# Kernel optimization log

Measured on AMD Instinct MI355X. Metric: run time of the kernel, lower is better.

The kernel has to match this reference:

```python
import jax, jax.numpy as jnp
import numpy as np

D_MODEL = 1024
N_HEADS = 16
D_HEAD = D_MODEL // N_HEADS
RANK = 128
N_COMPRESS = 64
STATE_DIM = 64
B_SZ = 2
S_LEN = 2048


def setup_inputs() -> dict:
    key = jax.random.key(0)
    ks = jax.random.split(key, 12)
    x = jax.random.normal(ks[0], (B_SZ, S_LEN, D_MODEL), dtype=jnp.float32)
    A = jax.random.normal(ks[1], (STATE_DIM, STATE_DIM), dtype=jnp.float32) * 0.01
    B_ssm = jax.random.normal(ks[2], (D_MODEL, STATE_DIM), dtype=jnp.float32) * 0.01
    W_imp = jax.random.normal(ks[3], (D_MODEL, STATE_DIM), dtype=jnp.float32) * 0.02   # Linear(state_dim->d_model), weight [out,in]
    W_router = jax.random.normal(ks[4], (N_COMPRESS, D_MODEL), dtype=jnp.float32) * 0.02
    compress_neurons = jax.random.normal(ks[5], (N_COMPRESS, D_MODEL, RANK), dtype=jnp.float32) * 0.02
    Wq = jax.random.normal(ks[6], (D_MODEL, RANK), dtype=jnp.float32) * 0.02
    Wk = jax.random.normal(ks[7], (D_MODEL, RANK), dtype=jnp.float32) * 0.02
    Wv = jax.random.normal(ks[8], (D_MODEL, RANK), dtype=jnp.float32) * 0.02
    Wo = jax.random.normal(ks[9], (D_MODEL, D_MODEL), dtype=jnp.float32) * 0.02
    mask = jnp.tril(jnp.ones((S_LEN, S_LEN), dtype=bool))[None, None]  # [1,1,S,S] causal
    return {"x": x, "A": A, "B_ssm": B_ssm, "W_imp": W_imp, "W_router": W_router,
            "compress_neurons": compress_neurons, "Wq": Wq, "Wk": Wk, "Wv": Wv,
            "Wo": Wo, "mask": mask}


def reference(x, A, B_ssm, W_imp, W_router, compress_neurons, Wq, Wk, Wv, Wo, mask):
    Bn, S, D = x.shape
    # ---- SSM: h_t = h_{t-1} @ A + x_t @ B (only final state is used) ----
    xB = jnp.einsum('bsd,dn->bsn', x, B_ssm)  # precompute input projection

    def step(h, u):
        h = h @ A + u
        return h, None

    h0 = jnp.zeros((Bn, STATE_DIM), dtype=x.dtype)
    h_final, _ = jax.lax.scan(step, h0, jnp.swapaxes(xB, 0, 1))  # scan over S

    h_proj = h_final @ W_imp.T                       # [B, d_model]
    importance = jax.nn.softmax(jnp.einsum('bsd,bd->bs', x, h_proj), axis=-1)

    # ---- Routing ----
    token_pref = jax.nn.softmax(x @ W_router.T, axis=-1)          # [B,S,n_compress]
    nw = jnp.einsum('bs,bsn->bn', importance, token_pref)         # [B,n_compress]
    nw = nw / (nw.sum(axis=-1, keepdims=True) + 1e-8)

    # ---- Shared compression -> QKV ----
    shared_compress = jnp.einsum('bn,ndr->bdr', nw, compress_neurons)  # [B,D,rank]
    hcomp = jnp.einsum('bsd,bdr->bsr', x, shared_compress)             # [B,S,rank]
    Q = (hcomp @ Wq.T).reshape(Bn, S, N_HEADS, D_HEAD).transpose(0, 2, 1, 3)
    K = (hcomp @ Wk.T).reshape(Bn, S, N_HEADS, D_HEAD).transpose(0, 2, 1, 3)
    V = (hcomp @ Wv.T).reshape(Bn, S, N_HEADS, D_HEAD).transpose(0, 2, 1, 3)

    scores = jnp.einsum('bhqd,bhkd->bhqk', Q, K) / np.sqrt(D_HEAD).astype(x.dtype)
    scores = jnp.where(mask, scores, jnp.array(-jnp.inf, dtype=scores.dtype))
    attn = jax.nn.softmax(scores, axis=-1)
    attn_out = jnp.einsum('bhqk,bhkd->bhqd', attn, V)
    attn_out = attn_out.transpose(0, 2, 1, 3).reshape(Bn, S, D_MODEL)
    output = attn_out @ Wo.T
    return output
```

## Files before the change

### kernel.cpp

```cpp
#include <hip/hip_runtime.h>
#include <hip/hip_bf16.h>

typedef __bf16 bf16x8 __attribute__((ext_vector_type(8)));
typedef float  f32x4  __attribute__((ext_vector_type(4)));
typedef float  f32x16 __attribute__((ext_vector_type(16)));
typedef unsigned int uint4v __attribute__((ext_vector_type(4)));

__device__ __forceinline__ unsigned short f2bf(float f){
  union { float f; unsigned int u; } v; v.f = f;
  unsigned int r = (v.u + 0x7FFFu + ((v.u >> 16) & 1u)) >> 16;
  return (unsigned short)r;
}

__device__ __forceinline__ float bf2f(unsigned short u){
  union { unsigned int i; float f; } v; v.i = ((unsigned int)u) << 16; return v.f;
}

__device__ __forceinline__ unsigned pkbf(float a, float b){
  unsigned r;
  asm("v_cvt_pk_bf16_f32 %0, %1, %2" : "=v"(r) : "v"(a), "v"(b));
  return r;
}

__device__ __forceinline__ void gload_lds16(const void* g, void* l){
  __builtin_amdgcn_global_load_lds(
      (const __attribute__((address_space(1))) unsigned int*)g,
      (__attribute__((address_space(3))) unsigned int*)l, 16, 0, 0);
}

#define MFMA16(a,b,c) __builtin_amdgcn_mfma_f32_16x16x32_bf16((a),(b),(c),0,0,0)
#define MFMA32(a,b,c) __builtin_amdgcn_mfma_f32_32x32x16_bf16((a),(b),(c),0,0,0)

__global__ void k_conv(const float* __restrict__ x,
                       const float* __restrict__ Wq, const float* __restrict__ Wk,
                       const float* __restrict__ Wv, const float* __restrict__ Wo,
                       const float* __restrict__ Wr,
                       unsigned short* __restrict__ xb16,
                       unsigned short* __restrict__ wqkv, unsigned short* __restrict__ wo,
                       unsigned short* __restrict__ wrt){
  int bid = blockIdx.x;
  if (bid < 4096){
    int i = (bid * 256 + threadIdx.x) * 4;
    float4 v = *reinterpret_cast<const float4*>(x + i);
    ushort4 r; r.x = f2bf(v.x); r.y = f2bf(v.y); r.z = f2bf(v.z); r.w = f2bf(v.w);
    *reinterpret_cast<ushort4*>(xb16 + i) = r;
    return;
  }
  int j = ((bid - 4096) * 256 + threadIdx.x) * 4;
  if (j < 393216){
    const float* s;
    if (j < 131072) s = Wq + j; else if (j < 262144) s = Wk + (j - 131072); else s = Wv + (j - 262144);
    float4 v = *reinterpret_cast<const float4*>(s);
    ushort4 r; r.x = f2bf(v.x); r.y = f2bf(v.y); r.z = f2bf(v.z); r.w = f2bf(v.w);
    *reinterpret_cast<ushort4*>(wqkv + j) = r;
  } else if (j < 1441792){
    int jj = j - 393216;
    float4 v = *reinterpret_cast<const float4*>(Wo + jj);
    ushort4 r; r.x = f2bf(v.x); r.y = f2bf(v.y); r.z = f2bf(v.z); r.w = f2bf(v.w);
    *reinterpret_cast<ushort4*>(wo + jj) = r;
  } else {
    int jj = j - 1441792;
    int n = jj >> 10, d = jj & 1023;
    ushort4 r;
    if (n < 64){
      float4 v = *reinterpret_cast<const float4*>(Wr + n * 1024 + d);
      r.x = f2bf(v.x); r.y = f2bf(v.y); r.z = f2bf(v.z); r.w = f2bf(v.w);
    } else { r.x = 0; r.y = 0; r.z = 0; r.w = 0; }
    *reinterpret_cast<ushort4*>(wrt + jj) = r;
  }
}

template<int CBF16>
__global__ __launch_bounds__(256) void k_gemm(
    const unsigned short* __restrict__ A, const unsigned short* __restrict__ Bt,
    void* __restrict__ Cv, int M, int N, int K,
    long sA, long sB, long sC)
{
  __shared__ __align__(16) unsigned short Al[128 * 64];
  __shared__ __align__(16) unsigned short Bl[128 * 64];
  const int tid = threadIdx.x, wv = tid >> 6, lane = tid & 63;
  const int bm = blockIdx.y * 128, bn = blockIdx.x * 128, z = blockIdx.z;
  const unsigned short* Ab = A + (long)z * sA;
  const unsigned short* Bb = Bt + (long)z * sB;
  const f32x4 zero = {0.f, 0.f, 0.f, 0.f};
  f32x4 acc[4][4];
  #pragma unroll
  for (int i = 0; i < 4; ++i)
    #pragma unroll
    for (int j = 0; j < 4; ++j) acc[i][j] = zero;
  const int mo = (wv & 1) * 64, no = (wv >> 1) * 64;

  for (int k0 = 0; k0 < K; k0 += 64){
    __syncthreads();
    #pragma unroll
    for (int i = 0; i < 4; ++i){
      int rr = (wv * 4 + i) * 8 + (lane >> 3);
      gload_lds16(Ab + (long)(bm + rr) * K + k0 + (lane & 7) * 8, &Al[(wv * 4 + i) * 8 * 64]);
      gload_lds16(Bb + (long)(bn + rr) * K + k0 + (lane & 7) * 8, &Bl[(wv * 4 + i) * 8 * 64]);
    }
    __syncthreads();
    #pragma unroll
    for (int ks = 0; ks < 2; ++ks){
      bf16x8 af[4], bfr[4];
      #pragma unroll
      for (int mi = 0; mi < 4; ++mi)
        af[mi] = *reinterpret_cast<const bf16x8*>(&Al[(mo + mi * 16 + (lane & 15)) * 64 + ks * 32 + (lane >> 4) * 8]);
      #pragma unroll
      for (int ni = 0; ni < 4; ++ni)
        bfr[ni] = *reinterpret_cast<const bf16x8*>(&Bl[(no + ni * 16 + (lane & 15)) * 64 + ks * 32 + (lane >> 4) * 8]);
      #pragma unroll
      for (int mi = 0; mi < 4; ++mi)
        #pragma unroll
        for (int ni = 0; ni < 4; ++ni)
          acc[mi][ni] = MFMA16(af[mi], bfr[ni], acc[mi][ni]);
    }
  }

  #pragma unroll
  for (int mi = 0; mi < 4; ++mi)
    #pragma unroll
    for (int ni = 0; ni < 4; ++ni)
      #pragma unroll
      for (int r = 0; r < 4; ++r){
        int row = bm + mo + mi * 16 + (lane >> 4) * 4 + r;
        int col = bn + no + ni * 16 + (lane & 15);
        float v = acc[mi][ni][r];
        if (CBF16) ((unsigned short*)Cv)[(long)z * sC + (long)row * N + col] = f2bf(v);
        else       ((float*)Cv)[(long)z * sC + (long)row * N + col] = v;
      }
}

__global__ __launch_bounds__(256) void k_gemm64(
    const unsigned short* __restrict__ A, const unsigned short* __restrict__ Bt,
    float* __restrict__ C, int M, int N, int K)
{
  __shared__ __align__(16) unsigned short Al[128 * 64];
  __shared__ __align__(16) unsigned short Bl[64 * 64];
  const int tid = threadIdx.x, wv = tid >> 6, lane = tid & 63;
  const int bm = blockIdx.y * 128, bn = blockIdx.x * 64;
  const f32x4 zero = {0.f, 0.f, 0.f, 0.f};
  f32x4 acc[4][2];
  #pragma unroll
  for (int i = 0; i < 4; ++i){ acc[i][0] = zero; acc[i][1] = zero; }
  const int mo = (wv & 1) * 64, no = (wv >> 1) * 32;

  for (int k0 = 0; k0 < K; k0 += 64){
    __syncthreads();
    #pragma unroll
    for (int i = 0; i < 4; ++i){
      int rr = (wv * 4 + i) * 8 + (lane >> 3);
      gload_lds16(A + (long)(bm + rr) * K + k0 + (lane & 7) * 8, &Al[(wv * 4 + i) * 8 * 64]);
    }
    #pragma unroll
    for (int i = 0; i < 2; ++i){
      int rr = (wv * 2 + i) * 8 + (lane >> 3);
      gload_lds16(Bt + (long)(bn + rr) * K + k0 + (lane & 7) * 8, &Bl[(wv * 2 + i) * 8 * 64]);
    }
    __syncthreads();
    #pragma unroll
    for (int ks = 0; ks < 2; ++ks){
      bf16x8 af[4], bfr[2];
      #pragma unroll
      for (int mi = 0; mi < 4; ++mi)
        af[mi] = *reinterpret_cast<const bf16x8*>(&Al[(mo + mi * 16 + (lane & 15)) * 64 + ks * 32 + (lane >> 4) * 8]);
      #pragma unroll
      for (int ni = 0; ni < 2; ++ni)
        bfr[ni] = *reinterpret_cast<const bf16x8*>(&Bl[(no + ni * 16 + (lane & 15)) * 64 + ks * 32 + (lane >> 4) * 8]);
      #pragma unroll
      for (int mi = 0; mi < 4; ++mi)
        #pragma unroll
        for (int ni = 0; ni < 2; ++ni)
          acc[mi][ni] = MFMA16(af[mi], bfr[ni], acc[mi][ni]);
    }
  }

  #pragma unroll
  for (int mi = 0; mi < 4; ++mi)
    #pragma unroll
    for (int ni = 0; ni < 2; ++ni)
      #pragma unroll
      for (int r = 0; r < 4; ++r){
        int row = bm + mo + mi * 16 + (lane >> 4) * 4 + r;
        int col = bn + no + ni * 16 + (lane & 15);
        C[(long)row * N + col] = acc[mi][ni][r];
      }
}

__global__ __launch_bounds__(256) void k_gemmsk(
    const unsigned short* __restrict__ A, const unsigned short* __restrict__ Bt,
    float* __restrict__ P, int M, int N, int Kfull, int KS,
    long sA, long sB)
{
  __shared__ __align__(16) unsigned short Al[128 * 64];
  __shared__ __align__(16) unsigned short Bl[128 * 64];
  const int tid = threadIdx.x, wv = tid >> 6, lane = tid & 63;
  const int bm = blockIdx.y * 128, bn = blockIdx.x * 128, z = blockIdx.z;
  const int b = z >> 2, s = z & 3;
  const unsigned short* Ab = A + (long)b * sA;
  const unsigned short* Bb = Bt + (long)b * sB;
  float* Pb = P + (long)z * M * N;
  const f32x4 zero = {0.f, 0.f, 0.f, 0.f};
  f32x4 acc[4][4];
  #pragma unroll
  for (int i = 0; i < 4; ++i)
    #pragma unroll
    for (int j = 0; j < 4; ++j) acc[i][j] = zero;
  const int mo = (wv & 1) * 64, no = (wv >> 1) * 64;

  const int k1 = s * KS + KS;
  for (int k0 = s * KS; k0 < k1; k0 += 64){
    __syncthreads();
    #pragma unroll
    for (int i = 0; i < 4; ++i){
      int rr = (wv * 4 + i) * 8 + (lane >> 3);
      gload_lds16(Ab + (long)(bm + rr) * Kfull + k0 + (lane & 7) * 8, &Al[(wv * 4 + i) * 8 * 64]);
      gload_lds16(Bb + (long)(bn + rr) * Kfull + k0 + (lane & 7) * 8, &Bl[(wv * 4 + i) * 8 * 64]);
    }
    __syncthreads();
    #pragma unroll
    for (int ks = 0; ks < 2; ++ks){
      bf16x8 af[4], bfr[4];
      #pragma unroll
      for (int mi = 0; mi < 4; ++mi)
        af[mi] = *reinterpret_cast<const bf16x8*>(&Al[(mo + mi * 16 + (lane & 15)) * 64 + ks * 32 + (lane >> 4) * 8]);
      #pragma unroll
      for (int ni = 0; ni < 4; ++ni)
        bfr[ni] = *reinterpret_cast<const bf16x8*>(&Bl[(no + ni * 16 + (lane & 15)) * 64 + ks * 32 + (lane >> 4) * 8]);
      #pragma unroll
      for (int mi = 0; mi < 4; ++mi)
        #pragma unroll
        for (int ni = 0; ni < 4; ++ni)
          acc[mi][ni] = MFMA16(af[mi], bfr[ni], acc[mi][ni]);
    }
  }

  #pragma unroll
  for (int mi = 0; mi < 4; ++mi)
    #pragma unroll
    for (int ni = 0; ni < 4; ++ni)
      #pragma unroll
      for (int r = 0; r < 4; ++r){
        int row = bm + mo + mi * 16 + (lane >> 4) * 4 + r;
        int col = bn + no + ni * 16 + (lane & 15);
        Pb[(long)row * N + col] = acc[mi][ni][r];
      }
}

__global__ __launch_bounds__(256) void k_hred(const float* __restrict__ hpp,
                                              unsigned short* __restrict__ hcomp){
  int i4 = (blockIdx.x * 256 + threadIdx.x) * 4;
  int b = i4 >> 18;
  int rem = i4 & 262143;
  const float* p = hpp + (long)(b * 4) * 262144 + rem;
  f32x4 v = *reinterpret_cast<const f32x4*>(p);
  v += *reinterpret_cast<const f32x4*>(p + 262144);
  v += *reinterpret_cast<const f32x4*>(p + 524288);
  v += *reinterpret_cast<const f32x4*>(p + 786432);
  ushort4 o; o.x = f2bf(v[0]); o.y = f2bf(v[1]); o.z = f2bf(v[2]); o.w = f2bf(v[3]);
  *reinterpret_cast<ushort4*>(hcomp + (long)b * 262144 + rem) = o;
}

__global__ __launch_bounds__(256) void k_xbt(const float* __restrict__ x, const float* __restrict__ Bs,
                                             float* __restrict__ xbt){
  int b = blockIdx.x >> 5, t = blockIdx.x & 31;
  int tid = threadIdx.x, n = tid & 63, p = tid >> 6;
  const float* xr = x + ((long)b * 2048 + 2016 + t) * 1024 + p * 256;
  const float* Bp = Bs + (p * 256) * 64 + n;
  float a0 = 0.f, a1 = 0.f, a2 = 0.f, a3 = 0.f;
  #pragma unroll 4
  for (int d = 0; d < 256; d += 4){
    float4 xv = *reinterpret_cast<const float4*>(xr + d);
    a0 += xv.x * Bp[(d    ) * 64];
    a1 += xv.y * Bp[(d + 1) * 64];
    a2 += xv.z * Bp[(d + 2) * 64];
    a3 += xv.w * Bp[(d + 3) * 64];
  }
  __shared__ float red[4][64];
  red[p][n] = (a0 + a1) + (a2 + a3);
  __syncthreads();
  if (tid < 64){
    float s = red[0][tid] + red[1][tid] + red[2][tid] + red[3][tid];
    xbt[(b * 32 + t) * 64 + tid] = s;
  }
}

__global__ void k_scan(const float* __restrict__ xbt, const float* __restrict__ A,
                       float* __restrict__ hfin){
  int b = blockIdx.x, j = threadIdx.x;
  float Ac[64];
  #pragma unroll
  for (int i = 0; i < 64; ++i) Ac[i] = A[i * 64 + j];
  __shared__ float xs[32][64];
  __shared__ float hs[64];
  #pragma unroll
  for (int t = 0; t < 32; ++t) xs[t][j] = xbt[(b * 32 + t) * 64 + j];
  hs[j] = xs[0][j];
  __syncthreads();
  for (int t = 1; t < 32; ++t){
    float a0 = 0.f, a1 = 0.f, a2 = 0.f, a3 = 0.f;
    #pragma unroll
    for (int ii = 0; ii < 16; ++ii){
      float4 h4 = *reinterpret_cast<const float4*>(&hs[ii * 4]);
      a0 += h4.x * Ac[ii * 4 + 0];
      a1 += h4.y * Ac[ii * 4 + 1];
      a2 += h4.z * Ac[ii * 4 + 2];
      a3 += h4.w * Ac[ii * 4 + 3];
    }
    float acc = (a0 + a1) + (a2 + a3) + xs[t][j];
    __syncthreads();
    hs[j] = acc;
    __syncthreads();
  }
  hfin[b * 64 + j] = hs[j];
}

__global__ __launch_bounds__(256) void k_hproj(const float* __restrict__ hfin,
                                               const float* __restrict__ Wimp,
                                               float* __restrict__ hproj){
  int bid = blockIdx.x;
  int b = bid >> 2;
  int d = (bid & 3) * 256 + threadIdx.x;
  __shared__ float hs[64];
  if (threadIdx.x < 64) hs[threadIdx.x] = hfin[b * 64 + threadIdx.x];
  __syncthreads();
  const float* wr = Wimp + (long)d * 64;
  float a0 = 0.f, a1 = 0.f, a2 = 0.f, a3 = 0.f;
  #pragma unroll
  for (int k = 0; k < 64; k += 4){
    float4 w4 = *reinterpret_cast<const float4*>(wr + k);
    float4 h4 = *reinterpret_cast<const float4*>(&hs[k]);
    a0 += w4.x * h4.x; a1 += w4.y * h4.y; a2 += w4.z * h4.z; a3 += w4.w * h4.w;
  }
  hproj[b * 1024 + d] = (a0 + a1) + (a2 + a3);
}

__global__ void k_logits(const float* __restrict__ x, const float* __restrict__ hproj,
                         float* __restrict__ l){
  int tid = threadIdx.x, lane = tid & 63, wv = tid >> 6;
  int rowbase = blockIdx.x * 16;
  int b = rowbase >> 11;
  float hp[16];
  #pragma unroll
  for (int i = 0; i < 16; ++i) hp[i] = hproj[b * 1024 + i * 64 + lane];
  for (int rr = 0; rr < 4; ++rr){
    int row = rowbase + wv * 4 + rr;
    const float* xr = x + (long)row * 1024;
    float acc = 0.f;
    #pragma unroll
    for (int i = 0; i < 16; ++i) acc += xr[i * 64 + lane] * hp[i];
    #pragma unroll
    for (int o = 32; o; o >>= 1) acc += __shfl_xor(acc, o, 64);
    if (lane == 0) l[row] = acc;
  }
}

__global__ void k_nwpart(const float* __restrict__ rpp, const float* __restrict__ lbuf,
                         float* __restrict__ nwp){
  int bid = blockIdx.x; int b = bid >> 4, chunk = bid & 15;
  int tid = threadIdx.x, wv = tid >> 6, lane = tid & 63;
  __shared__ float wred[4], wsum[4];
  __shared__ float red[4][64];
  const float* lr = lbuf + b * 2048;
  float4 va = *reinterpret_cast<const float4*>(lr + tid * 8);
  float4 vb = *reinterpret_cast<const float4*>(lr + tid * 8 + 4);
  float mx8 = fmaxf(fmaxf(fmaxf(va.x, va.y), fmaxf(va.z, va.w)),
                    fmaxf(fmaxf(vb.x, vb.y), fmaxf(vb.z, vb.w)));
  #pragma unroll
  for (int o = 32; o; o >>= 1) mx8 = fmaxf(mx8, __shfl_xor(mx8, o, 64));
  if (lane == 0) wred[wv] = mx8;
  __syncthreads();
  float M = fmaxf(fmaxf(wred[0], wred[1]), fmaxf(wred[2], wred[3]));
  float se = __expf(va.x - M) + __expf(va.y - M) + __expf(va.z - M) + __expf(va.w - M)
           + __expf(vb.x - M) + __expf(vb.y - M) + __expf(vb.z - M) + __expf(vb.w - M);
  #pragma unroll
  for (int o = 32; o; o >>= 1) se += __shfl_xor(se, o, 64);
  if (lane == 0) wsum[wv] = se;
  __syncthreads();
  float inv = 1.f / (wsum[0] + wsum[1] + wsum[2] + wsum[3]);

  float accn = 0.f;
  for (int t = 0; t < 32; ++t){
    int s = chunk * 128 + wv * 32 + t;
    long off = ((long)b * 2048 + s) * 128 + lane;
    float v = rpp[off] + rpp[off + 524288] + rpp[off + 1048576] + rpp[off + 1572864];
    float mx = v;
    #pragma unroll
    for (int o = 32; o; o >>= 1) mx = fmaxf(mx, __shfl_xor(mx, o, 64));
    float e = __expf(v - mx);
    float sm = e;
    #pragma unroll
    for (int o = 32; o; o >>= 1) sm += __shfl_xor(sm, o, 64);
    float impv = __expf(lr[s] - M) * inv;
    accn += impv * (e / sm);
  }
  red[wv][lane] = accn;
  __syncthreads();
  if (wv == 0){
    float t = red[0][lane] + red[1][lane] + red[2][lane] + red[3][lane];
    nwp[bid * 64 + lane] = t;
  }
}

__global__ void k_sc(const float* __restrict__ cn, const float* __restrict__ nwp,
                     unsigned short* __restrict__ sct){
  int tid = threadIdx.x;
  long idx = (long)blockIdx.x * 256 + tid;
  int d = (int)(idx >> 5); int r0 = (int)(idx & 31) * 4;
  __shared__ float nws[128];
  if (tid < 128){
    int bb = tid >> 6, nn = tid & 63;
    float a = 0.f;
    #pragma unroll
    for (int c = 0; c < 16; ++c) a += nwp[(bb * 16 + c) * 64 + nn];
    float tot = a;
    #pragma unroll
    for (int o = 32; o; o >>= 1) tot += __shfl_xor(tot, o, 64);
    nws[tid] = a / (tot + 1e-8f);
  }
  __syncthreads();
  f32x4 a0 = {0.f,0.f,0.f,0.f}, a1 = {0.f,0.f,0.f,0.f};
  for (int n = 0; n < 64; ++n){
    f32x4 c = *reinterpret_cast<const f32x4*>(&cn[((long)n * 1024 + d) * 128 + r0]);
    a0 += nws[n] * c;
    a1 += nws[64 + n] * c;
  }
  #pragma unroll
  for (int e = 0; e < 4; ++e){
    sct[(long)(r0 + e) * 1024 + d]        = f2bf(a0[e]);
    sct[(long)(128 + r0 + e) * 1024 + d]  = f2bf(a1[e]);
  }
}

__global__ __launch_bounds__(256, 4) void k_attn(const unsigned short* __restrict__ qkv,
                                                 unsigned short* __restrict__ Op,
                                                 float* __restrict__ ml,
                                                 int nspl, int nsh){
  __shared__ __align__(16) unsigned short KlA[64 * 64];
  __shared__ __align__(16) unsigned short VtA[64 * 64];
  char* Kl = (char*)KlA;
  char* Vt = (char*)VtA;
  const int tid = threadIdx.x, wq = tid >> 6, lane = tid & 63;
  const int l31 = lane & 31, hi = lane >> 5;
  const float CEXP = 0.18033688011112042f;

  int li = blockIdx.x;
  int j = li & 7, m = li >> 3;
  int g = j * 4 + (m & 3);
  int r5 = m >> 2;
  int k5 = r5 & 7, sel = r5 >> 3;
  int qb = (sel < nspl) ? (15 - k5) : k5;
  int part = (sel < nspl) ? sel : (sel - nspl);
  int h = g & 15, b = g >> 4;
  int pidx = (g * 16 + qb) * nspl + part;

  int T = 2 * qb + 2;
  int t0 = (part * T) >> nsh;
  int t1 = ((part + 1) * T) >> nsh;

  int qbase = qb * 128 + wq * 32;
  int KTw = qbase >> 6;
  const unsigned short* base = qkv + (long)b * 2048 * 3072;

  bf16x8 qf[4];
  #pragma unroll
  for (int i = 0; i < 4; ++i)
    qf[i] = *reinterpret_cast<const bf16x8*>(base + (long)(qbase + l31) * 3072 + h * 64 + i * 16 + hi * 8);

  f32x16 oacc[2];
  #pragma unroll
  for (int d = 0; d < 2; ++d)
    #pragma unroll
    for (int r = 0; r < 16; ++r) oacc[d][r] = 0.f;
  float m_r = -3.0e38f, l_r = 0.f;

  for (int kt = t0; kt < t1; ++kt){
    #pragma unroll
    for (int it = 0; it < 2; ++it){
      int key = it * 32 + wq * 8 + (lane >> 3);
      int sc = (lane & 7) ^ (key & 7);
      gload_lds16(base + (long)(kt * 64 + key) * 3072 + 1024 + h * 64 + sc * 8,
                  Kl + (it * 32 + wq * 8) * 128);
    }
    #pragma unroll
    for (int it = 0; it < 2; ++it){
      int dhg = wq + it * 4;
      uint4 vvv = *reinterpret_cast<const uint4*>(base + (long)(kt * 64 + lane) * 3072 + 2048 + h * 64 + dhg * 8);
      const unsigned short* vs = reinterpret_cast<const unsigned short*>(&vvv);
      #pragma unroll
      for (int e = 0; e < 8; ++e){
        int dh = dhg * 8 + e;
        *reinterpret_cast<unsigned short*>(Vt + dh * 128 + ((((lane >> 3) ^ (dh & 7))) << 4) + (lane & 7) * 2) = vs[e];
      }
    }
    __syncthreads();

    if (kt <= KTw){
      bool diag = (kt == KTw);

      f32x16 sa[2];
      __builtin_amdgcn_s_setprio(1);
      #pragma unroll
      for (int kb = 0; kb < 2; ++kb){
        #pragma unroll
        for (int r = 0; r < 16; ++r) sa[kb][r] = 0.f;
        int row = kb * 32 + l31;
        #pragma unroll
        for (int i2 = 0; i2 < 4; ++i2){
          bf16x8 kf = *reinterpret_cast<const bf16x8*>(
              Kl + row * 128 + ((((i2 << 1) | hi) ^ (l31 & 7)) << 4));
          sa[kb] = MFMA32(kf, qf[i2], sa[kb]);
        }
      }
      __builtin_amdgcn_s_setprio(0);

      float pv[32];
      #pragma unroll
      for (int kb = 0; kb < 2; ++kb)
        #pragma unroll
        for (int r = 0; r < 16; ++r) pv[kb * 16 + r] = sa[kb][r];

      if (diag){
        int qg = qbase + l31;
        #pragma unroll
        for (int kb = 0; kb < 2; ++kb)
          #pragma unroll
          for (int r = 0; r < 16; ++r){
            int kg = kt * 64 + kb * 32 + (r & 3) + ((r >> 2) << 3) + (hi << 2);
            if (kg > qg) pv[kb * 16 + r] = -3.0e38f;
          }
      }

      float mx = pv[0];
      #pragma unroll
      for (int r = 1; r < 32; ++r) mx = fmaxf(mx, pv[r]);
      mx = fmaxf(mx, __shfl_xor(mx, 32, 64));

      float scl;
      if (__all(mx <= m_r + 44.0f)){
        scl = 1.f;
      } else {
        float mnew = fmaxf(m_r, mx);
        scl = exp2f((m_r - mnew) * CEXP);
        m_r = mnew;
        #pragma unroll
        for (int d = 0; d < 2; ++d)
          #pragma unroll
          for (int r = 0; r < 16; ++r) oacc[d][r] *= scl;
      }
      float mn_c = m_r * CEXP;
      float rs = 0.f;
      #pragma unroll
      for (int r = 0; r < 32; ++r){
        float e = exp2f(__builtin_fmaf(pv[r], CEXP, -mn_c));
        pv[r] = e; rs += e;
      }
      rs += __shfl_xor(rs, 32, 64);
      l_r = l_r * scl + rs;

      bf16x8 pa[4];
      #pragma unroll
      for (int kb = 0; kb < 2; ++kb){
        unsigned W[4][2], X[4][2];
        #pragma unroll
        for (int u = 0; u < 4; ++u){
          W[u][0] = pkbf(pv[kb * 16 + 4 * u + 0], pv[kb * 16 + 4 * u + 1]);
          W[u][1] = pkbf(pv[kb * 16 + 4 * u + 2], pv[kb * 16 + 4 * u + 3]);
        }
        #pragma unroll
        for (int u = 0; u < 4; ++u){
          X[u][0] = (unsigned)__shfl_xor((int)W[u][0], 32, 64);
          X[u][1] = (unsigned)__shfl_xor((int)W[u][1], 32, 64);
        }
        #pragma unroll
        for (int t2 = 0; t2 < 2; ++t2){
          int u0 = 2 * t2, u1 = u0 + 1;
          uint4v wt;
          wt.x = hi ? X[u1][0] : W[u0][0];
          wt.y = hi ? X[u1][1] : W[u0][1];
          wt.z = hi ? W[u1][0] : X[u0][0];
          wt.w = hi ? W[u1][1] : X[u0][1];
          pa[kb * 2 + t2] = __builtin_bit_cast(bf16x8, wt);
        }
      }
      __builtin_amdgcn_s_setprio(1);
      #pragma unroll
      for (int db = 0; db < 2; ++db){
        int row = db * 32 + l31;
        #pragma unroll
        for (int t = 0; t < 4; ++t){
          bf16x8 vf = *reinterpret_cast<const bf16x8*>(
              Vt + row * 128 + ((((t << 1) | hi) ^ (l31 & 7)) << 4));
          oacc[db] = MFMA32(vf, pa[t], oacc[db]);
        }
      }
      __builtin_amdgcn_s_setprio(0);
    }
    __syncthreads();
  }

  unsigned short* Oq = Op + (long)pidx * 8192 + (wq * 32 + l31) * 64;
  #pragma unroll
  for (int db = 0; db < 2; ++db)
    #pragma unroll
    for (int r4 = 0; r4 < 4; ++r4){
      ushort4 o;
      o.x = f2bf(oacc[db][r4 * 4 + 0]);
      o.y = f2bf(oacc[db][r4 * 4 + 1]);
      o.z = f2bf(oacc[db][r4 * 4 + 2]);
      o.w = f2bf(oacc[db][r4 * 4 + 3]);
      *reinterpret_cast<ushort4*>(Oq + db * 32 + r4 * 8 + hi * 4) = o;
    }
  if (hi == 0){
    float2 v; v.x = m_r; v.y = l_r;
    *reinterpret_cast<float2*>(ml + ((long)pidx * 128 + wq * 32 + l31) * 2) = v;
  }
}

__global__ __launch_bounds__(256) void k_amerge(const unsigned short* __restrict__ Op,
                                                const float* __restrict__ ml,
                                                unsigned short* __restrict__ ao,
                                                int nspl){
  const float CEXP = 0.18033688011112042f;
  int mid = blockIdx.x;
  int g = mid >> 4, qb = mid & 15;
  int b = g >> 4, h = g & 15;
  const unsigned short* O0 = Op + (long)mid * nspl * 8192;
  const float* mlb = ml + (long)mid * nspl * 256;
  int t = threadIdx.x;
  #pragma unroll
  for (int i = 0; i < 8; ++i){
    int idx = i * 256 + t;
    int q = idx >> 4, c4 = (idx & 15) * 4;
    float m0 = mlb[q * 2],       l0 = mlb[q * 2 + 1];
    float m1 = mlb[256 + q * 2], l1 = mlb[256 + q * 2 + 1];
    float m2 = -3.0e38f, l2 = 0.f, m3 = -3.0e38f, l3 = 0.f;
    if (nspl == 4){
      m2 = mlb[512 + q * 2]; l2 = mlb[512 + q * 2 + 1];
      m3 = mlb[768 + q * 2]; l3 = mlb[768 + q * 2 + 1];
    }
    float mm = fmaxf(fmaxf(m0, m1), fmaxf(m2, m3));
    float s0 = exp2f((m0 - mm) * CEXP), s1 = exp2f((m1 - mm) * CEXP);
    float s2 = exp2f((m2 - mm) * CEXP), s3 = exp2f((m3 - mm) * CEXP);
    float linv = 1.f / (l0 * s0 + l1 * s1 + l2 * s2 + l3 * s3);
    s0 *= linv; s1 *= linv; s2 *= linv; s3 *= linv;
    ushort4 a = *reinterpret_cast<const ushort4*>(O0 + q * 64 + c4);
    ushort4 c = *reinterpret_cast<const ushort4*>(O0 + 8192 + q * 64 + c4);
    ushort4 a2 = {0,0,0,0}, a3 = {0,0,0,0};
    if (nspl == 4){
      a2 = *reinterpret_cast<const ushort4*>(O0 + 16384 + q * 64 + c4);
      a3 = *reinterpret_cast<const ushort4*>(O0 + 24576 + q * 64 + c4);
    }
    ushort4 o;
    o.x = f2bf(bf2f(a.x) * s0 + bf2f(c.x) * s1 + bf2f(a2.x) * s2 + bf2f(a3.x) * s3);
    o.y = f2bf(bf2f(a.y) * s0 + bf2f(c.y) * s1 + bf2f(a2.y) * s2 + bf2f(a3.y) * s3);
    o.z = f2bf(bf2f(a.z) * s0 + bf2f(c.z) * s1 + bf2f(a2.z) * s2 + bf2f(a3.z) * s3);
    o.w = f2bf(bf2f(a.w) * s0 + bf2f(c.w) * s1 + bf2f(a2.w) * s2 + bf2f(a3.w) * s3);
    *reinterpret_cast<ushort4*>(ao + ((long)b * 2048 + qb * 128 + q) * 1024 + h * 64 + c4) = o;
  }
}

extern "C" void kernel_launch(void* const* d_in, const int* in_sizes, int n_in,
                              void* d_out, int out_size, void* d_ws, size_t ws_size,
                              hipStream_t stream){
  (void)in_sizes; (void)n_in; (void)out_size;
  const float* x    = (const float*)d_in[0];
  const float* A    = (const float*)d_in[1];
  const float* Bs   = (const float*)d_in[2];
  const float* Wimp = (const float*)d_in[3];
  const float* Wr   = (const float*)d_in[4];
  const float* cn   = (const float*)d_in[5];
  const float* Wq   = (const float*)d_in[6];
  const float* Wk   = (const float*)d_in[7];
  const float* Wv   = (const float*)d_in[8];
  const float* Wo   = (const float*)d_in[9];
  float* out = (float*)d_out;
  char* ws = (char*)d_ws;

  int nspl, nsh;
  {
    size_t tot4 = (size_t)512*4*16384 + (size_t)512*4*1024 + 25165824 + 2097152 + 2800000;
    if (ws_size >= tot4){ nspl = 4; nsh = 2; } else { nspl = 2; nsh = 1; }
  }
  size_t opart_b = (size_t)512 * nspl * 16384;
  size_t ml_off  = opart_b;
  size_t qkv_off = ml_off + (size_t)512 * nspl * 1024;
  size_t wo_off  = qkv_off + 25165824;
  size_t ext     = wo_off + 2097152;

  unsigned short* Opart = (unsigned short*)(ws);
  float*          mlbuf = (float*)(ws + ml_off);
  unsigned short* qkvb  = (unsigned short*)(ws + qkv_off);
  float*          hpp   = (float*)(ws + qkv_off);
  unsigned short* aob   = (unsigned short*)(ws + qkv_off);
  unsigned short* wo_t  = (unsigned short*)(ws + wo_off);
  unsigned short* xb16  = (unsigned short*)(ws + 0);
  float*          rpp   = (float*)(ws + 8388608);
  unsigned short* sct   = (unsigned short*)(ws + ext);
  float*          xbt   = (float*)(ws + ext + 524288);
  float*          hproj = (float*)(ws + ext + 540672);
  float*          lbuf  = (float*)(ws + ext + 548864);
  float*          nwp   = (float*)(ws + ext + 565248);
  float*          hfin  = (float*)(ws + ext + 573440);
  unsigned short* wqkv  = (unsigned short*)(ws + ext + 577536);
  unsigned short* wrt   = (unsigned short*)(ws + ext + 1363968);
  unsigned short* hcomp = (unsigned short*)(ws + ext + 1626112);

  k_conv<<<5632, 256, 0, stream>>>(x, Wq, Wk, Wv, Wo, Wr, xb16, wqkv, wo_t, wrt);
  k_gemmsk<<<dim3(1, 32, 4), 256, 0, stream>>>(xb16, wrt, rpp, 4096, 128, 1024, 256, 0, 0);
  k_xbt<<<64, 256, 0, stream>>>(x, Bs, xbt);
  k_scan<<<2, 64, 0, stream>>>(xbt, A, hfin);
  k_hproj<<<8, 256, 0, stream>>>(hfin, Wimp, hproj);
  k_logits<<<256, 256, 0, stream>>>(x, hproj, lbuf);
  k_nwpart<<<32, 256, 0, stream>>>(rpp, lbuf, nwp);
  k_sc<<<128, 256, 0, stream>>>(cn, nwp, sct);
  k_gemmsk<<<dim3(1, 16, 8), 256, 0, stream>>>(xb16, sct, hpp, 2048, 128, 1024, 256,
                                               2048L * 1024, 128L * 1024);
  k_hred<<<512, 256, 0, stream>>>(hpp, hcomp);
  k_gemm<1><<<dim3(24, 16, 2), 256, 0, stream>>>(hcomp, wqkv, qkvb, 2048, 3072, 128,
                                                 2048L * 128, 0, 2048L * 3072);
  k_attn<<<dim3(512 * nspl), 256, 0, stream>>>(qkvb, Opart, mlbuf, nspl, nsh);
  k_amerge<<<dim3(512), 256, 0, stream>>>(Opart, mlbuf, aob, nspl);
  k_gemm64<<<dim3(16, 32), 256, 0, stream>>>(aob, wo_t, out, 4096, 1024, 1024);
}
```

Before: 199.3 us.

## Fold SSM projection and scan into existing kernels, tree-reduce softmax, split merge

```diff
diff --git a/kernel.cpp b/kernel.cpp
--- a/kernel.cpp
+++ b/kernel.cpp
@@ -34,11 +34,34 @@
 __global__ void k_conv(const float* __restrict__ x,
                        const float* __restrict__ Wq, const float* __restrict__ Wk,
                        const float* __restrict__ Wv, const float* __restrict__ Wo,
-                       const float* __restrict__ Wr,
+                       const float* __restrict__ Wr, const float* __restrict__ Bs,
                        unsigned short* __restrict__ xb16,
                        unsigned short* __restrict__ wqkv, unsigned short* __restrict__ wo,
-                       unsigned short* __restrict__ wrt){
+                       unsigned short* __restrict__ wrt, float* __restrict__ xbt){
   int bid = blockIdx.x;
+  if (bid >= 5632){
+    int bb = (bid - 5632) >> 5, t = (bid - 5632) & 31;
+    int tid = threadIdx.x, n = tid & 63, p = tid >> 6;
+    const float* xr = x + ((long)bb * 2048 + 2016 + t) * 1024 + p * 256;
+    const float* Bp = Bs + (p * 256) * 64 + n;
+    float a0 = 0.f, a1 = 0.f, a2 = 0.f, a3 = 0.f;
+    #pragma unroll 4
+    for (int d = 0; d < 256; d += 4){
+      float4 xv = *reinterpret_cast<const float4*>(xr + d);
+      a0 += xv.x * Bp[(d    ) * 64];
+      a1 += xv.y * Bp[(d + 1) * 64];
+      a2 += xv.z * Bp[(d + 2) * 64];
+      a3 += xv.w * Bp[(d + 3) * 64];
+    }
+    __shared__ float red[4][64];
+    red[p][n] = (a0 + a1) + (a2 + a3);
+    __syncthreads();
+    if (tid < 64){
+      float s = red[0][tid] + red[1][tid] + red[2][tid] + red[3][tid];
+      xbt[(bb * 32 + t) * 64 + tid] = s;
+    }
+    return;
+  }
   if (bid < 4096){
     int i = (bid * 256 + threadIdx.x) * 4;
     float4 v = *reinterpret_cast<const float4*>(x + i);
@@ -189,11 +212,42 @@
 __global__ __launch_bounds__(256) void k_gemmsk(
     const unsigned short* __restrict__ A, const unsigned short* __restrict__ Bt,
     float* __restrict__ P, int M, int N, int Kfull, int KS,
-    long sA, long sB)
+    long sA, long sB,
+    int do_scan, const float* __restrict__ xbt, const float* __restrict__ Asc,
+    float* __restrict__ hfin)
 {
   __shared__ __align__(16) unsigned short Al[128 * 64];
   __shared__ __align__(16) unsigned short Bl[128 * 64];
   const int tid = threadIdx.x, wv = tid >> 6, lane = tid & 63;
+
+  if (do_scan && blockIdx.z == 4){
+    if (blockIdx.y < 2 && tid < 64){
+      int b = blockIdx.y, j = tid;
+      float Ac[64];
+      #pragma unroll
+      for (int i = 0; i < 64; ++i) Ac[i] = Asc[i * 64 + j];
+      float* xs = (float*)Al;
+      float* hs = xs + 2048;
+      #pragma unroll
+      for (int t = 0; t < 32; ++t) xs[t * 64 + j] = xbt[(b * 32 + t) * 64 + j];
+      hs[j] = xs[j];
+      for (int t = 1; t < 32; ++t){
+        float a0 = 0.f, a1 = 0.f, a2 = 0.f, a3 = 0.f;
+        #pragma unroll
+        for (int ii = 0; ii < 16; ++ii){
+          float4 h4 = *reinterpret_cast<const float4*>(&hs[ii * 4]);
+          a0 += h4.x * Ac[ii * 4 + 0];
+          a1 += h4.y * Ac[ii * 4 + 1];
+          a2 += h4.z * Ac[ii * 4 + 2];
+          a3 += h4.w * Ac[ii * 4 + 3];
+        }
+        hs[j] = (a0 + a1) + (a2 + a3) + xs[t * 64 + j];
+      }
+      hfin[b * 64 + j] = hs[j];
+    }
+    return;
+  }
+
   const int bm = blockIdx.y * 128, bn = blockIdx.x * 128, z = blockIdx.z;
   const int b = z >> 2, s = z & 3;
   const unsigned short* Ab = A + (long)b * sA;
@@ -260,60 +314,6 @@
   *reinterpret_cast<ushort4*>(hcomp + (long)b * 262144 + rem) = o;
 }
 
-__global__ __launch_bounds__(256) void k_xbt(const float* __restrict__ x, const float* __restrict__ Bs,
-                                             float* __restrict__ xbt){
-  int b = blockIdx.x >> 5, t = blockIdx.x & 31;
-  int tid = threadIdx.x, n = tid & 63, p = tid >> 6;
-  const float* xr = x + ((long)b * 2048 + 2016 + t) * 1024 + p * 256;
-  const float* Bp = Bs + (p * 256) * 64 + n;
-  float a0 = 0.f, a1 = 0.f, a2 = 0.f, a3 = 0.f;
-  #pragma unroll 4
-  for (int d = 0; d < 256; d += 4){
-    float4 xv = *reinterpret_cast<const float4*>(xr + d);
-    a0 += xv.x * Bp[(d    ) * 64];
-    a1 += xv.y * Bp[(d + 1) * 64];
-    a2 += xv.z * Bp[(d + 2) * 64];
-    a3 += xv.w * Bp[(d + 3) * 64];
-  }
-  __shared__ float red[4][64];
-  red[p][n] = (a0 + a1) + (a2 + a3);
-  __syncthreads();
-  if (tid < 64){
-    float s = red[0][tid] + red[1][tid] + red[2][tid] + red[3][tid];
-    xbt[(b * 32 + t) * 64 + tid] = s;
-  }
-}
-
-__global__ void k_scan(const float* __restrict__ xbt, const float* __restrict__ A,
-                       float* __restrict__ hfin){
-  int b = blockIdx.x, j = threadIdx.x;
-  float Ac[64];
-  #pragma unroll
-  for (int i = 0; i < 64; ++i) Ac[i] = A[i * 64 + j];
-  __shared__ float xs[32][64];
-  __shared__ float hs[64];
-  #pragma unroll
-  for (int t = 0; t < 32; ++t) xs[t][j] = xbt[(b * 32 + t) * 64 + j];
-  hs[j] = xs[0][j];
-  __syncthreads();
-  for (int t = 1; t < 32; ++t){
-    float a0 = 0.f, a1 = 0.f, a2 = 0.f, a3 = 0.f;
-    #pragma unroll
-    for (int ii = 0; ii < 16; ++ii){
-      float4 h4 = *reinterpret_cast<const float4*>(&hs[ii * 4]);
-      a0 += h4.x * Ac[ii * 4 + 0];
-      a1 += h4.y * Ac[ii * 4 + 1];
-      a2 += h4.z * Ac[ii * 4 + 2];
-      a3 += h4.w * Ac[ii * 4 + 3];
-    }
-    float acc = (a0 + a1) + (a2 + a3) + xs[t][j];
-    __syncthreads();
-    hs[j] = acc;
-    __syncthreads();
-  }
-  hfin[b * 64 + j] = hs[j];
-}
-
 __global__ __launch_bounds__(256) void k_hproj(const float* __restrict__ hfin,
                                                const float* __restrict__ Wimp,
                                                float* __restrict__ hproj){
@@ -530,9 +530,14 @@
           }
       }
 
-      float mx = pv[0];
-      #pragma unroll
-      for (int r = 1; r < 32; ++r) mx = fmaxf(mx, pv[r]);
+      float mt[16];
+      #pragma unroll
+      for (int r = 0; r < 16; ++r) mt[r] = fmaxf(pv[r], pv[r + 16]);
+      #pragma unroll
+      for (int r = 0; r < 8; ++r) mt[r] = fmaxf(mt[r], mt[r + 8]);
+      #pragma unroll
+      for (int r = 0; r < 4; ++r) mt[r] = fmaxf(mt[r], mt[r + 4]);
+      float mx = fmaxf(fmaxf(mt[0], mt[1]), fmaxf(mt[2], mt[3]));
       mx = fmaxf(mx, __shfl_xor(mx, 32, 64));
 
       float scl;
@@ -548,12 +553,15 @@
           for (int r = 0; r < 16; ++r) oacc[d][r] *= scl;
       }
       float mn_c = m_r * CEXP;
-      float rs = 0.f;
-      #pragma unroll
-      for (int r = 0; r < 32; ++r){
-        float e = exp2f(__builtin_fmaf(pv[r], CEXP, -mn_c));
-        pv[r] = e; rs += e;
-      }
+      float rs0 = 0.f, rs1 = 0.f, rs2 = 0.f, rs3 = 0.f;
+      #pragma unroll
+      for (int r = 0; r < 32; r += 4){
+        float e0 = exp2f(__builtin_fmaf(pv[r    ], CEXP, -mn_c)); pv[r    ] = e0; rs0 += e0;
+        float e1 = exp2f(__builtin_fmaf(pv[r + 1], CEXP, -mn_c)); pv[r + 1] = e1; rs1 += e1;
+        float e2 = exp2f(__builtin_fmaf(pv[r + 2], CEXP, -mn_c)); pv[r + 2] = e2; rs2 += e2;
+        float e3 = exp2f(__builtin_fmaf(pv[r + 3], CEXP, -mn_c)); pv[r + 3] = e3; rs3 += e3;
+      }
+      float rs = (rs0 + rs1) + (rs2 + rs3);
       rs += __shfl_xor(rs, 32, 64);
       l_r = l_r * scl + rs;
 
@@ -621,15 +629,16 @@
                                                 unsigned short* __restrict__ ao,
                                                 int nspl){
   const float CEXP = 0.18033688011112042f;
-  int mid = blockIdx.x;
+  int mid = blockIdx.x >> 1;
+  int hh = blockIdx.x & 1;
   int g = mid >> 4, qb = mid & 15;
   int b = g >> 4, h = g & 15;
   const unsigned short* O0 = Op + (long)mid * nspl * 8192;
   const float* mlb = ml + (long)mid * nspl * 256;
   int t = threadIdx.x;
   #pragma unroll
-  for (int i = 0; i < 8; ++i){
-    int idx = i * 256 + t;
+  for (int i = 0; i < 4; ++i){
+    int idx = hh * 1024 + i * 256 + t;
     int q = idx >> 4, c4 = (idx & 15) * 4;
     float m0 = mlb[q * 2],       l0 = mlb[q * 2 + 1];
     float m1 = mlb[256 + q * 2], l1 = mlb[256 + q * 2 + 1];
@@ -705,20 +714,19 @@
   unsigned short* wrt   = (unsigned short*)(ws + ext + 1363968);
   unsigned short* hcomp = (unsigned short*)(ws + ext + 1626112);
 
-  k_conv<<<5632, 256, 0, stream>>>(x, Wq, Wk, Wv, Wo, Wr, xb16, wqkv, wo_t, wrt);
-  k_gemmsk<<<dim3(1, 32, 4), 256, 0, stream>>>(xb16, wrt, rpp, 4096, 128, 1024, 256, 0, 0);
-  k_xbt<<<64, 256, 0, stream>>>(x, Bs, xbt);
-  k_scan<<<2, 64, 0, stream>>>(xbt, A, hfin);
+  k_conv<<<5696, 256, 0, stream>>>(x, Wq, Wk, Wv, Wo, Wr, Bs, xb16, wqkv, wo_t, wrt, xbt);
+  k_gemmsk<<<dim3(1, 32, 5), 256, 0, stream>>>(xb16, wrt, rpp, 4096, 128, 1024, 256, 0, 0,
+                                               1, xbt, A, hfin);
   k_hproj<<<8, 256, 0, stream>>>(hfin, Wimp, hproj);
   k_logits<<<256, 256, 0, stream>>>(x, hproj, lbuf);
   k_nwpart<<<32, 256, 0, stream>>>(rpp, lbuf, nwp);
   k_sc<<<128, 256, 0, stream>>>(cn, nwp, sct);
   k_gemmsk<<<dim3(1, 16, 8), 256, 0, stream>>>(xb16, sct, hpp, 2048, 128, 1024, 256,
-                                               2048L * 1024, 128L * 1024);
+                                               2048L * 1024, 128L * 1024, 0, nullptr, nullptr, nullptr);
   k_hred<<<512, 256, 0, stream>>>(hpp, hcomp);
   k_gemm<1><<<dim3(24, 16, 2), 256, 0, stream>>>(hcomp, wqkv, qkvb, 2048, 3072, 128,
                                                  2048L * 128, 0, 2048L * 3072);
   k_attn<<<dim3(512 * nspl), 256, 0, stream>>>(qkvb, Opart, mlbuf, nspl, nsh);
-  k_amerge<<<dim3(512), 256, 0, stream>>>(Opart, mlbuf, aob, nspl);
+  k_amerge<<<dim3(1024), 256, 0, stream>>>(Opart, mlbuf, aob, nspl);
   k_gemm64<<<dim3(16, 32), 256, 0, stream>>>(aob, wo_t, out, 4096, 1024, 1024);
 }
```

Result: faster. 169.4 us (-15.0%).
